# Kernel optimization log

Measured on AMD Instinct MI355X. Metric: run time of the kernel, lower is better.

Reference implementation:

```python
import jax, jax.numpy as jnp
import numpy as np
import math

N, L, C, H, K = 4, 16384, 256, 8, 4
D = C // H


def setup_inputs():
    rng = jax.random.key(0)
    ks = jax.random.split(rng, 16)
    def w(k, shape, scale):
        return jax.random.normal(k, shape, jnp.float32) * scale
    s = 1.0 / math.sqrt(C)
    return {
        "query": jax.random.normal(ks[0], (N, L, C), jnp.float32),
        "key": jax.random.normal(ks[1], (N, L, C), jnp.float32),
        "value": jax.random.normal(ks[2], (N, L, C), jnp.float32),
        "reference_points": jax.random.uniform(ks[3], (N, L, 2), jnp.float32),
        "pos_embed": jax.random.normal(ks[4], (N, L, C), jnp.float32),
        "Wq": w(ks[5], (C, C), s), "bq": jnp.zeros((C,), jnp.float32),
        "Wk": w(ks[6], (C, C), s), "bk": jnp.zeros((C,), jnp.float32),
        "Wv": w(ks[7], (C, C), s), "bv": jnp.zeros((C,), jnp.float32),
        "Wo1": w(ks[8], (C, 2 * C), s), "bo1": jnp.zeros((2 * C,), jnp.float32),
        "Wo2": w(ks[9], (2 * C, H * K * 2), 0.02), "bo2": w(ks[10], (H * K * 2,), 0.02),
        "Wpos": w(ks[11], (C, C), s), "bpos": jnp.zeros((C,), jnp.float32),
        "Wout": w(ks[12], (C, C), s), "bout": jnp.zeros((C,), jnp.float32),
    }


def _sample_weight(points):
    # F.grid_sample on a 1x1 feature map (bilinear, zeros padding, align_corners=False)
    # degenerates to a scalar weight: grid g = 2p-1, unnormalized c = g/2 = p - 0.5,
    # pixel-0 bilinear weight per axis = max(0, 1 - |c|).
    c = points - 0.5
    return jax.nn.relu(1.0 - jnp.abs(c[..., 0])) * jax.nn.relu(1.0 - jnp.abs(c[..., 1]))


def reference(query, key, value, reference_points, pos_embed,
              Wq, bq, Wk, bk, Wv, bv, Wo1, bo1, Wo2, bo2, Wpos, bpos, Wout, bout):
    Nb, Ln, Cd = query.shape
    q = (query @ Wq + bq).reshape(Nb, Ln, H, D)
    k = (key @ Wk + bk).reshape(Nb, Ln, H, D)
    v = (value @ Wv + bv).reshape(Nb, Ln, H, D)
    pos = (pos_embed @ Wpos + bpos).reshape(Nb, Ln, H, D)
    q = q + pos
    k = k + pos
    # offset MLP: Linear(C,2C) -> ReLU -> Linear(2C, H*K*2)
    offsets = (jax.nn.relu(query @ Wo1 + bo1) @ Wo2 + bo2).reshape(Nb, Ln, H, K, 2)
    sp = reference_points[:, :, None, None, :] + offsets  # [N,L,H,K,2]
    w = _sample_weight(sp)                                # [N,L,H,K]
    # sampled_k[n,l,h,k,:] = k[n,l,h,:] * w[n,l,h,k]  (1x1 grid_sample closed form)
    qk = jnp.einsum('nlhd,nlhd->nlh', q, k)               # [N,L,H]
    attn = jax.nn.softmax(qk[..., None] * w / math.sqrt(D), axis=-1)  # [N,L,H,K]
    # output = sum_k attn_k * (v * w_k) = v * sum_k(attn_k * w_k)
    wv = jnp.sum(attn * w, axis=-1)                       # [N,L,H]
    out = (v * wv[..., None]).reshape(Nb, Ln, Cd)
    return out @ Wout + bout
```

## Files before the change

kernel.cpp:

```cpp
#include <hip/hip_runtime.h>
#include <hip/hip_bf16.h>

typedef __bf16 bf16x8 __attribute__((ext_vector_type(8)));
typedef float f32x4 __attribute__((ext_vector_type(4)));
typedef float f32x2 __attribute__((ext_vector_type(2)));

#define MT 64
#define CC 256

__device__ __forceinline__ void barrier_lds() {
    __builtin_amdgcn_sched_barrier(0);
    asm volatile("s_waitcnt lgkmcnt(0)" ::: "memory");
    __builtin_amdgcn_s_barrier();
    __builtin_amdgcn_sched_barrier(0);
}

__device__ __forceinline__ int swz(int r, int c) {
    return r * 512 + ((c * 2) ^ ((r & 7) << 4));
}

__device__ __forceinline__ bf16x8 ldB(const __bf16* __restrict__ WT, int nc, int KC, int kc,
                                      int laneoff) {
    return *(const bf16x8*)(WT + ((size_t)nc * KC + kc) * 512 + laneoff);
}

__device__ __forceinline__ void stream_tile(const float* __restrict__ src, int row0, int tid,
                                            __bf16* dst) {
#pragma unroll
    for (int i = 0; i < 8; ++i) {
        int f = i * 512 + tid;
        int r = f >> 6;
        int c = (f & 63) * 4;
        f32x4 v = __builtin_nontemporal_load((const f32x4*)(src + (size_t)(row0 + r) * CC + c));
        union { __bf16 h[4]; unsigned long long u; } uu;
        uu.h[0] = (__bf16)v[0]; uu.h[1] = (__bf16)v[1];
        uu.h[2] = (__bf16)v[2]; uu.h[3] = (__bf16)v[3];
        *(unsigned long long*)((char*)dst + swz(r, c)) = uu.u;
    }
}

__global__ void prep_all(const float* __restrict__ Wq, const float* __restrict__ Wk,
                         const float* __restrict__ Wpos, const float* __restrict__ Wo1,
                         const float* __restrict__ Wo2, const float* __restrict__ Wv,
                         const float* __restrict__ Wout, __bf16* __restrict__ ws)
{
    int i = blockIdx.x * 256 + threadIdx.x;
    if (i >= 557056) return;
    int j, K, N;
    const float* S0 = nullptr; const float* S1 = nullptr;
    if (i < 131072)      { j = i;          K = 512; N = 256; S0 = Wq;  S1 = Wpos; }
    else if (i < 262144) { j = i - 131072; K = 512; N = 256; S0 = Wk;  S1 = Wpos; }
    else if (i < 393216) { j = i - 262144; K = 256; N = 512; S0 = Wo1; }
    else if (i < 425984) { j = i - 393216; K = 512; N = 64;  S0 = Wo2; }
    else if (i < 491520) { j = i - 425984; K = 256; N = 256; S0 = Wv; }
    else                 { j = i - 491520; K = 256; N = 256; S0 = Wout; }
    int tile = j >> 9, r = j & 511;
    int lane = r >> 3, e = r & 7;
    int q4 = lane >> 4, r16 = lane & 15;
    int KC = K >> 5;
    int nc = tile / KC, kc = tile - nc * KC;
    int k = kc * 32 + q4 * 8 + e;
    int n = nc * 16 + r16;
    float v;
    if (S1 && k >= 256) v = S1[(size_t)(k - 256) * N + n];
    else                v = S0[(size_t)k * N + n];
    ws[i] = (__bf16)v;
}

extern "C" __global__ void __launch_bounds__(512, 2)
fused_ext_attn(const float* __restrict__ query, const float* __restrict__ key,
               const float* __restrict__ value, const float* __restrict__ refp,
               const float* __restrict__ pose,
               const __bf16* __restrict__ ws,
               const float* __restrict__ bq, const float* __restrict__ bk,
               const float* __restrict__ bv, const float* __restrict__ bpos,
               const float* __restrict__ bo1, const float* __restrict__ bo2,
               const float* __restrict__ bout,
               float* __restrict__ out)
{
    const __bf16* WTqp  = ws;
    const __bf16* WTkp  = ws + 131072;
    const __bf16* WTo1  = ws + 262144;
    const __bf16* WTo2  = ws + 393216;
    const __bf16* WTv   = ws + 425984;
    const __bf16* WTout = ws + 491520;

    __shared__ __attribute__((aligned(16))) __bf16 SA[MT * CC];
    __shared__ __attribute__((aligned(16))) __bf16 SX[MT * CC];
    __shared__ __attribute__((aligned(16))) char   SY[12288];

    __bf16* off_b = (__bf16*)SY;
    float*  qk_s  = (float*)(SY + 8192);
    float*  wv_s  = (float*)(SY + 10240);

    const int tid = threadIdx.x;
    const int lane = tid & 63;
    const int wid = tid >> 6;
    const int r16 = lane & 15;
    const int q4 = lane >> 4;
    const int laneoff = lane * 8;
    const int row0 = blockIdx.x * MT;

    stream_tile(query, row0, tid, SA);
    barrier_lds();

    f32x4 accO[4];
#pragma unroll
    for (int i = 0; i < 4; ++i) accO[i] = (f32x4){0.f, 0.f, 0.f, 0.f};
    for (int p = 0; p < 2; ++p) {
        f32x4 acc[4][2];
#pragma unroll
        for (int i = 0; i < 4; ++i)
#pragma unroll
            for (int j = 0; j < 2; ++j) acc[i][j] = (f32x4){0.f, 0.f, 0.f, 0.f};
#pragma unroll
        for (int ks = 0; ks < 8; ++ks) {
            int ak = ks * 32 + q4 * 8;
            bf16x8 a[4], b[2];
#pragma unroll
            for (int mf = 0; mf < 4; ++mf)
                a[mf] = *(const bf16x8*)((const char*)SA + swz(mf * 16 + r16, ak));
#pragma unroll
            for (int nf = 0; nf < 2; ++nf)
                b[nf] = ldB(WTo1, p * 16 + wid * 2 + nf, 8, ks, laneoff);
#pragma unroll
            for (int mf = 0; mf < 4; ++mf)
#pragma unroll
                for (int nf = 0; nf < 2; ++nf)
                    acc[mf][nf] = __builtin_amdgcn_mfma_f32_16x16x32_bf16(a[mf], b[nf], acc[mf][nf], 0, 0, 0);
        }
#pragma unroll
        for (int mf = 0; mf < 4; ++mf)
#pragma unroll
            for (int nf = 0; nf < 2; ++nf) {
                int col = wid * 32 + nf * 16 + r16;
                float bias = bo1[p * 256 + col];
#pragma unroll
                for (int r = 0; r < 4; ++r)
                    *(__bf16*)((char*)SX + swz(mf * 16 + q4 * 4 + r, col)) =
                        (__bf16)fmaxf(acc[mf][nf][r] + bias, 0.f);
            }
        barrier_lds();
        if (wid < 4) {
#pragma unroll
            for (int ks = 0; ks < 8; ++ks) {
                int ak = ks * 32 + q4 * 8;
                bf16x8 b = ldB(WTo2, wid, 16, p * 8 + ks, laneoff);
#pragma unroll
                for (int mf = 0; mf < 4; ++mf) {
                    bf16x8 a = *(const bf16x8*)((const char*)SX + swz(mf * 16 + r16, ak));
                    accO[mf] = __builtin_amdgcn_mfma_f32_16x16x32_bf16(a, b, accO[mf], 0, 0, 0);
                }
            }
            if (p == 1) {
                int col = wid * 16 + r16;
                float b2 = bo2[col];
#pragma unroll
                for (int mf = 0; mf < 4; ++mf)
#pragma unroll
                    for (int r = 0; r < 4; ++r)
                        off_b[(mf * 16 + q4 * 4 + r) * 64 + col] = (__bf16)(accO[mf][r] + b2);
            }
        }
        barrier_lds();
    }

    f32x4 qa[4][2];
#pragma unroll
    for (int i = 0; i < 4; ++i)
#pragma unroll
        for (int j = 0; j < 2; ++j) qa[i][j] = (f32x4){0.f, 0.f, 0.f, 0.f};
    stream_tile(pose, row0, tid, SX);
#pragma unroll
    for (int ks = 0; ks < 8; ++ks) {
        int ak = ks * 32 + q4 * 8;
        bf16x8 a[4], b[2];
#pragma unroll
        for (int mf = 0; mf < 4; ++mf)
            a[mf] = *(const bf16x8*)((const char*)SA + swz(mf * 16 + r16, ak));
#pragma unroll
        for (int nf = 0; nf < 2; ++nf)
            b[nf] = ldB(WTqp, wid * 2 + nf, 16, ks, laneoff);
#pragma unroll
        for (int mf = 0; mf < 4; ++mf)
#pragma unroll
            for (int nf = 0; nf < 2; ++nf)
                qa[mf][nf] = __builtin_amdgcn_mfma_f32_16x16x32_bf16(a[mf], b[nf], qa[mf][nf], 0, 0, 0);
    }
    barrier_lds();

    stream_tile(key, row0, tid, SA);
#pragma unroll
    for (int ks = 8; ks < 16; ++ks) {
        int ak = (ks - 8) * 32 + q4 * 8;
        bf16x8 a[4], b[2];
#pragma unroll
        for (int mf = 0; mf < 4; ++mf)
            a[mf] = *(const bf16x8*)((const char*)SX + swz(mf * 16 + r16, ak));
#pragma unroll
        for (int nf = 0; nf < 2; ++nf)
            b[nf] = ldB(WTqp, wid * 2 + nf, 16, ks, laneoff);
#pragma unroll
        for (int mf = 0; mf < 4; ++mf)
#pragma unroll
            for (int nf = 0; nf < 2; ++nf)
                qa[mf][nf] = __builtin_amdgcn_mfma_f32_16x16x32_bf16(a[mf], b[nf], qa[mf][nf], 0, 0, 0);
    }
    barrier_lds();

    {
        f32x4 ka[4][2];
#pragma unroll
        for (int i = 0; i < 4; ++i)
#pragma unroll
            for (int j = 0; j < 2; ++j) ka[i][j] = (f32x4){0.f, 0.f, 0.f, 0.f};
#pragma unroll
        for (int ks = 0; ks < 16; ++ks) {
            int ak = (ks & 7) * 32 + q4 * 8;
            const char* Abase = (ks < 8) ? (const char*)SA : (const char*)SX;
            bf16x8 a[4], b[2];
#pragma unroll
            for (int mf = 0; mf < 4; ++mf)
                a[mf] = *(const bf16x8*)(Abase + swz(mf * 16 + r16, ak));
#pragma unroll
            for (int nf = 0; nf < 2; ++nf)
                b[nf] = ldB(WTkp, wid * 2 + nf, 16, ks, laneoff);
#pragma unroll
            for (int mf = 0; mf < 4; ++mf)
#pragma unroll
                for (int nf = 0; nf < 2; ++nf)
                    ka[mf][nf] = __builtin_amdgcn_mfma_f32_16x16x32_bf16(a[mf], b[nf], ka[mf][nf], 0, 0, 0);
        }
        float Bq[2], Bk[2];
#pragma unroll
        for (int nf = 0; nf < 2; ++nf) {
            int col = wid * 32 + nf * 16 + r16;
            Bq[nf] = bq[col] + bpos[col];
            Bk[nf] = bk[col] + bpos[col];
        }
#pragma unroll
        for (int mf = 0; mf < 4; ++mf)
#pragma unroll
            for (int r = 0; r < 4; ++r) {
                float p0 = (qa[mf][0][r] + Bq[0]) * (ka[mf][0][r] + Bk[0])
                         + (qa[mf][1][r] + Bq[1]) * (ka[mf][1][r] + Bk[1]);
#pragma unroll
                for (int m = 1; m < 16; m <<= 1)
                    p0 += __shfl_xor(p0, m);
                if (r16 == 0)
                    qk_s[(mf * 16 + q4 * 4 + r) * 8 + wid] = p0;
            }
    }
    barrier_lds();

    stream_tile(value, row0, tid, SA);
    {
        int t = tid >> 3, h = tid & 7;
        float qk = qk_s[t * 8 + h];
        f32x2 rp = __builtin_nontemporal_load((const f32x2*)(refp + (size_t)(row0 + t) * 2));
        float wgt[4], lg[4];
        float m = -1e30f;
#pragma unroll
        for (int kk = 0; kk < 4; ++kk) {
            float ox = (float)off_b[t * 64 + (h * 4 + kk) * 2];
            float oy = (float)off_b[t * 64 + (h * 4 + kk) * 2 + 1];
            float cx = rp[0] + ox - 0.5f, cy = rp[1] + oy - 0.5f;
            float wx = fmaxf(0.f, 1.f - fabsf(cx));
            float wy = fmaxf(0.f, 1.f - fabsf(cy));
            wgt[kk] = wx * wy;
            lg[kk] = qk * wgt[kk] * 0.17677669529663687f;
            m = fmaxf(m, lg[kk]);
        }
        float s = 0.f, sw = 0.f;
#pragma unroll
        for (int kk = 0; kk < 4; ++kk) {
            float e = __expf(lg[kk] - m);
            s += e;
            sw += e * wgt[kk];
        }
        wv_s[t * 8 + h] = sw / s;
    }
    barrier_lds();

    {
        f32x4 acc[4][2];
#pragma unroll
        for (int i = 0; i < 4; ++i)
#pragma unroll
            for (int j = 0; j < 2; ++j) acc[i][j] = (f32x4){0.f, 0.f, 0.f, 0.f};
#pragma unroll
        for (int ks = 0; ks < 8; ++ks) {
            int ak = ks * 32 + q4 * 8;
            bf16x8 a[4], b[2];
#pragma unroll
            for (int mf = 0; mf < 4; ++mf)
                a[mf] = *(const bf16x8*)((const char*)SA + swz(mf * 16 + r16, ak));
#pragma unroll
            for (int nf = 0; nf < 2; ++nf)
                b[nf] = ldB(WTv, wid * 2 + nf, 8, ks, laneoff);
#pragma unroll
            for (int mf = 0; mf < 4; ++mf)
#pragma unroll
                for (int nf = 0; nf < 2; ++nf)
                    acc[mf][nf] = __builtin_amdgcn_mfma_f32_16x16x32_bf16(a[mf], b[nf], acc[mf][nf], 0, 0, 0);
        }
#pragma unroll
        for (int mf = 0; mf < 4; ++mf)
#pragma unroll
            for (int nf = 0; nf < 2; ++nf) {
                int col = wid * 32 + nf * 16 + r16;
                float bias = bv[col];
#pragma unroll
                for (int r = 0; r < 4; ++r) {
                    int row = mf * 16 + q4 * 4 + r;
                    float wvv = wv_s[row * 8 + wid];
                    *(__bf16*)((char*)SX + swz(row, col)) = (__bf16)((acc[mf][nf][r] + bias) * wvv);
                }
            }
    }
    barrier_lds();

    {
        f32x4 acc[4][2];
#pragma unroll
        for (int i = 0; i < 4; ++i)
#pragma unroll
            for (int j = 0; j < 2; ++j) acc[i][j] = (f32x4){0.f, 0.f, 0.f, 0.f};
#pragma unroll
        for (int ks = 0; ks < 8; ++ks) {
            int ak = ks * 32 + q4 * 8;
            bf16x8 a[4], b[2];
#pragma unroll
            for (int mf = 0; mf < 4; ++mf)
                a[mf] = *(const bf16x8*)((const char*)SX + swz(mf * 16 + r16, ak));
#pragma unroll
            for (int nf = 0; nf < 2; ++nf)
                b[nf] = ldB(WTout, wid * 2 + nf, 8, ks, laneoff);
#pragma unroll
            for (int mf = 0; mf < 4; ++mf)
#pragma unroll
                for (int nf = 0; nf < 2; ++nf)
                    acc[mf][nf] = __builtin_amdgcn_mfma_f32_16x16x32_bf16(a[mf], b[nf], acc[mf][nf], 0, 0, 0);
        }
#pragma unroll
        for (int mf = 0; mf < 4; ++mf)
#pragma unroll
            for (int nf = 0; nf < 2; ++nf) {
                int col = wid * 32 + nf * 16 + r16;
                float bias = bout[col];
#pragma unroll
                for (int r = 0; r < 4; ++r) {
                    int row = mf * 16 + q4 * 4 + r;
                    __builtin_nontemporal_store(acc[mf][nf][r] + bias,
                                                out + (size_t)(row0 + row) * CC + col);
                }
            }
    }
}

extern "C" void kernel_launch(void* const* d_in, const int* in_sizes, int n_in,
                              void* d_out, int out_size, void* d_ws, size_t ws_size,
                              hipStream_t stream)
{
    const float* query = (const float*)d_in[0];
    const float* key   = (const float*)d_in[1];
    const float* value = (const float*)d_in[2];
    const float* refp  = (const float*)d_in[3];
    const float* pose  = (const float*)d_in[4];
    const float* Wq  = (const float*)d_in[5];  const float* bq   = (const float*)d_in[6];
    const float* Wk  = (const float*)d_in[7];  const float* bk   = (const float*)d_in[8];
    const float* Wv  = (const float*)d_in[9];  const float* bv   = (const float*)d_in[10];
    const float* Wo1 = (const float*)d_in[11]; const float* bo1  = (const float*)d_in[12];
    const float* Wo2 = (const float*)d_in[13]; const float* bo2  = (const float*)d_in[14];
    const float* Wpos= (const float*)d_in[15]; const float* bpos = (const float*)d_in[16];
    const float* Wout= (const float*)d_in[17]; const float* bout = (const float*)d_in[18];

    __bf16* ws = (__bf16*)d_ws;

    prep_all<<<2176, 256, 0, stream>>>(Wq, Wk, Wpos, Wo1, Wo2, Wv, Wout, ws);

    fused_ext_attn<<<65536 / MT, 512, 0, stream>>>(
        query, key, value, refp, pose, ws,
        bq, bk, bv, bpos, bo1, bo2, bout, (float*)d_out);
}
```

Before: 140.4 us.

## Prefetch next GEMM weight fragments into registers ahead of each stage

Each stage's weight B-fragments (a full 8x2 set of bf16x8 per wave) are now loaded into registers before the preceding barrier or right after the previous GEMM, so global weight loads overlap with LDS stores, barriers and the tile streaming. The offset-MLP loop is unrolled into explicit stages, with the second-layer weights preloaded. To hold the larger register footprint, launch bounds drop from 2 to 1 block per CU, which cuts occupancy and may expose latency elsewhere.

```diff
diff --git a/kernel.cpp b/kernel.cpp
--- a/kernel.cpp
+++ b/kernel.cpp
@@ -22,6 +22,38 @@
 __device__ __forceinline__ bf16x8 ldB(const __bf16* __restrict__ WT, int nc, int KC, int kc,
                                       int laneoff) {
     return *(const bf16x8*)(WT + ((size_t)nc * KC + kc) * 512 + laneoff);
+}
+
+__device__ __forceinline__ void pre16(bf16x8 (&d)[8][2], const __bf16* __restrict__ WT,
+                                      int nc0, int KC, int kc0, int laneoff) {
+#pragma unroll
+    for (int ks = 0; ks < 8; ++ks)
+#pragma unroll
+        for (int nf = 0; nf < 2; ++nf)
+            d[ks][nf] = ldB(WT, nc0 + nf, KC, kc0 + ks, laneoff);
+}
+__device__ __forceinline__ void pre8(bf16x8 (&d)[8], const __bf16* __restrict__ WT,
+                                     int nc, int KC, int kc0, int laneoff) {
+#pragma unroll
+    for (int ks = 0; ks < 8; ++ks)
+        d[ks] = ldB(WT, nc, KC, kc0 + ks, laneoff);
+}
+
+__device__ __forceinline__ void gemm16(const char* A, const bf16x8 (&b)[8][2],
+                                       f32x4 (&acc)[4][2], int r16, int q4) {
+#pragma unroll
+    for (int ks = 0; ks < 8; ++ks) {
+        int ak = ks * 32 + q4 * 8;
+        bf16x8 a[4];
+#pragma unroll
+        for (int mf = 0; mf < 4; ++mf)
+            a[mf] = *(const bf16x8*)(A + swz(mf * 16 + r16, ak));
+#pragma unroll
+        for (int mf = 0; mf < 4; ++mf)
+#pragma unroll
+            for (int nf = 0; nf < 2; ++nf)
+                acc[mf][nf] = __builtin_amdgcn_mfma_f32_16x16x32_bf16(a[mf], b[ks][nf], acc[mf][nf], 0, 0, 0);
+    }
 }
 
 __device__ __forceinline__ void stream_tile(const float* __restrict__ src, int row0, int tid,
@@ -67,7 +99,7 @@
     ws[i] = (__bf16)v;
 }
 
-extern "C" __global__ void __launch_bounds__(512, 2)
+extern "C" __global__ void __launch_bounds__(512, 1)
 fused_ext_attn(const float* __restrict__ query, const float* __restrict__ key,
                const float* __restrict__ value, const float* __restrict__ refp,
                const float* __restrict__ pose,
@@ -101,69 +133,94 @@
     const int laneoff = lane * 8;
     const int row0 = blockIdx.x * MT;
 
+    bf16x8 bh[8][2];
     stream_tile(query, row0, tid, SA);
+    pre16(bh, WTo1, wid * 2, 8, 0, laneoff);
     barrier_lds();
 
     f32x4 accO[4];
 #pragma unroll
     for (int i = 0; i < 4; ++i) accO[i] = (f32x4){0.f, 0.f, 0.f, 0.f};
-    for (int p = 0; p < 2; ++p) {
+    bf16x8 bo[8];
+    {
         f32x4 acc[4][2];
 #pragma unroll
         for (int i = 0; i < 4; ++i)
 #pragma unroll
             for (int j = 0; j < 2; ++j) acc[i][j] = (f32x4){0.f, 0.f, 0.f, 0.f};
-#pragma unroll
-        for (int ks = 0; ks < 8; ++ks) {
-            int ak = ks * 32 + q4 * 8;
-            bf16x8 a[4], b[2];
-#pragma unroll
-            for (int mf = 0; mf < 4; ++mf)
-                a[mf] = *(const bf16x8*)((const char*)SA + swz(mf * 16 + r16, ak));
-#pragma unroll
-            for (int nf = 0; nf < 2; ++nf)
-                b[nf] = ldB(WTo1, p * 16 + wid * 2 + nf, 8, ks, laneoff);
-#pragma unroll
-            for (int mf = 0; mf < 4; ++mf)
-#pragma unroll
-                for (int nf = 0; nf < 2; ++nf)
-                    acc[mf][nf] = __builtin_amdgcn_mfma_f32_16x16x32_bf16(a[mf], b[nf], acc[mf][nf], 0, 0, 0);
-        }
+        gemm16((const char*)SA, bh, acc, r16, q4);
+        pre8(bo, WTo2, wid & 3, 16, 0, laneoff);
 #pragma unroll
         for (int mf = 0; mf < 4; ++mf)
 #pragma unroll
             for (int nf = 0; nf < 2; ++nf) {
                 int col = wid * 32 + nf * 16 + r16;
-                float bias = bo1[p * 256 + col];
+                float bias = bo1[col];
 #pragma unroll
                 for (int r = 0; r < 4; ++r)
                     *(__bf16*)((char*)SX + swz(mf * 16 + q4 * 4 + r, col)) =
                         (__bf16)fmaxf(acc[mf][nf][r] + bias, 0.f);
             }
-        barrier_lds();
-        if (wid < 4) {
-#pragma unroll
-            for (int ks = 0; ks < 8; ++ks) {
-                int ak = ks * 32 + q4 * 8;
-                bf16x8 b = ldB(WTo2, wid, 16, p * 8 + ks, laneoff);
-#pragma unroll
-                for (int mf = 0; mf < 4; ++mf) {
-                    bf16x8 a = *(const bf16x8*)((const char*)SX + swz(mf * 16 + r16, ak));
-                    accO[mf] = __builtin_amdgcn_mfma_f32_16x16x32_bf16(a, b, accO[mf], 0, 0, 0);
-                }
-            }
-            if (p == 1) {
-                int col = wid * 16 + r16;
-                float b2 = bo2[col];
-#pragma unroll
-                for (int mf = 0; mf < 4; ++mf)
-#pragma unroll
-                    for (int r = 0; r < 4; ++r)
-                        off_b[(mf * 16 + q4 * 4 + r) * 64 + col] = (__bf16)(accO[mf][r] + b2);
-            }
-        }
-        barrier_lds();
-    }
+    }
+    barrier_lds();
+
+    if (wid < 4) {
+#pragma unroll
+        for (int ks = 0; ks < 8; ++ks) {
+            int ak = ks * 32 + q4 * 8;
+#pragma unroll
+            for (int mf = 0; mf < 4; ++mf) {
+                bf16x8 a = *(const bf16x8*)((const char*)SX + swz(mf * 16 + r16, ak));
+                accO[mf] = __builtin_amdgcn_mfma_f32_16x16x32_bf16(a, bo[ks], accO[mf], 0, 0, 0);
+            }
+        }
+    }
+    pre16(bh, WTo1, 16 + wid * 2, 8, 0, laneoff);
+    barrier_lds();
+
+    {
+        f32x4 acc[4][2];
+#pragma unroll
+        for (int i = 0; i < 4; ++i)
+#pragma unroll
+            for (int j = 0; j < 2; ++j) acc[i][j] = (f32x4){0.f, 0.f, 0.f, 0.f};
+        gemm16((const char*)SA, bh, acc, r16, q4);
+        pre8(bo, WTo2, wid & 3, 16, 8, laneoff);
+#pragma unroll
+        for (int mf = 0; mf < 4; ++mf)
+#pragma unroll
+            for (int nf = 0; nf < 2; ++nf) {
+                int col = wid * 32 + nf * 16 + r16;
+                float bias = bo1[256 + col];
+#pragma unroll
+                for (int r = 0; r < 4; ++r)
+                    *(__bf16*)((char*)SX + swz(mf * 16 + q4 * 4 + r, col)) =
+                        (__bf16)fmaxf(acc[mf][nf][r] + bias, 0.f);
+            }
+    }
+    barrier_lds();
+
+    bf16x8 bg[8][2];
+    if (wid < 4) {
+#pragma unroll
+        for (int ks = 0; ks < 8; ++ks) {
+            int ak = ks * 32 + q4 * 8;
+#pragma unroll
+            for (int mf = 0; mf < 4; ++mf) {
+                bf16x8 a = *(const bf16x8*)((const char*)SX + swz(mf * 16 + r16, ak));
+                accO[mf] = __builtin_amdgcn_mfma_f32_16x16x32_bf16(a, bo[ks], accO[mf], 0, 0, 0);
+            }
+        }
+        int col = (wid & 3) * 16 + r16;
+        float b2 = bo2[col];
+#pragma unroll
+        for (int mf = 0; mf < 4; ++mf)
+#pragma unroll
+            for (int r = 0; r < 4; ++r)
+                off_b[(mf * 16 + q4 * 4 + r) * 64 + col] = (__bf16)(accO[mf][r] + b2);
+    }
+    pre16(bg, WTqp, wid * 2, 16, 0, laneoff);
+    barrier_lds();
 
     f32x4 qa[4][2];
 #pragma unroll
@@ -171,41 +228,14 @@
 #pragma unroll
         for (int j = 0; j < 2; ++j) qa[i][j] = (f32x4){0.f, 0.f, 0.f, 0.f};
     stream_tile(pose, row0, tid, SX);
-#pragma unroll
-    for (int ks = 0; ks < 8; ++ks) {
-        int ak = ks * 32 + q4 * 8;
-        bf16x8 a[4], b[2];
-#pragma unroll
-        for (int mf = 0; mf < 4; ++mf)
-            a[mf] = *(const bf16x8*)((const char*)SA + swz(mf * 16 + r16, ak));
-#pragma unroll
-        for (int nf = 0; nf < 2; ++nf)
-            b[nf] = ldB(WTqp, wid * 2 + nf, 16, ks, laneoff);
-#pragma unroll
-        for (int mf = 0; mf < 4; ++mf)
-#pragma unroll
-            for (int nf = 0; nf < 2; ++nf)
-                qa[mf][nf] = __builtin_amdgcn_mfma_f32_16x16x32_bf16(a[mf], b[nf], qa[mf][nf], 0, 0, 0);
-    }
-    barrier_lds();
-
+    gemm16((const char*)SA, bg, qa, r16, q4);
+    pre16(bg, WTqp, wid * 2, 16, 8, laneoff);
+    barrier_lds();
+
+    bf16x8 bk1[8][2];
     stream_tile(key, row0, tid, SA);
-#pragma unroll
-    for (int ks = 8; ks < 16; ++ks) {
-        int ak = (ks - 8) * 32 + q4 * 8;
-        bf16x8 a[4], b[2];
-#pragma unroll
-        for (int mf = 0; mf < 4; ++mf)
-            a[mf] = *(const bf16x8*)((const char*)SX + swz(mf * 16 + r16, ak));
-#pragma unroll
-        for (int nf = 0; nf < 2; ++nf)
-            b[nf] = ldB(WTqp, wid * 2 + nf, 16, ks, laneoff);
-#pragma unroll
-        for (int mf = 0; mf < 4; ++mf)
-#pragma unroll
-            for (int nf = 0; nf < 2; ++nf)
-                qa[mf][nf] = __builtin_amdgcn_mfma_f32_16x16x32_bf16(a[mf], b[nf], qa[mf][nf], 0, 0, 0);
-    }
+    gemm16((const char*)SX, bg, qa, r16, q4);
+    pre16(bk1, WTkp, wid * 2, 16, 0, laneoff);
     barrier_lds();
 
     {
@@ -214,14 +244,14 @@
         for (int i = 0; i < 4; ++i)
 #pragma unroll
             for (int j = 0; j < 2; ++j) ka[i][j] = (f32x4){0.f, 0.f, 0.f, 0.f};
-#pragma unroll
-        for (int ks = 0; ks < 16; ++ks) {
-            int ak = (ks & 7) * 32 + q4 * 8;
-            const char* Abase = (ks < 8) ? (const char*)SA : (const char*)SX;
+        gemm16((const char*)SA, bk1, ka, r16, q4);
+#pragma unroll
+        for (int ks = 8; ks < 16; ++ks) {
+            int ak = (ks - 8) * 32 + q4 * 8;
             bf16x8 a[4], b[2];
 #pragma unroll
             for (int mf = 0; mf < 4; ++mf)
-                a[mf] = *(const bf16x8*)(Abase + swz(mf * 16 + r16, ak));
+                a[mf] = *(const bf16x8*)((const char*)SX + swz(mf * 16 + r16, ak));
 #pragma unroll
             for (int nf = 0; nf < 2; ++nf)
                 b[nf] = ldB(WTkp, wid * 2 + nf, 16, ks, laneoff);
@@ -231,6 +261,7 @@
                 for (int nf = 0; nf < 2; ++nf)
                     ka[mf][nf] = __builtin_amdgcn_mfma_f32_16x16x32_bf16(a[mf], b[nf], ka[mf][nf], 0, 0, 0);
         }
+        pre16(bg, WTv, wid * 2, 8, 0, laneoff);
         float Bq[2], Bk[2];
 #pragma unroll
         for (int nf = 0; nf < 2; ++nf) {
@@ -288,22 +319,8 @@
         for (int i = 0; i < 4; ++i)
 #pragma unroll
             for (int j = 0; j < 2; ++j) acc[i][j] = (f32x4){0.f, 0.f, 0.f, 0.f};
-#pragma unroll
-        for (int ks = 0; ks < 8; ++ks) {
-            int ak = ks * 32 + q4 * 8;
-            bf16x8 a[4], b[2];
-#pragma unroll
-            for (int mf = 0; mf < 4; ++mf)
-                a[mf] = *(const bf16x8*)((const char*)SA + swz(mf * 16 + r16, ak));
-#pragma unroll
-            for (int nf = 0; nf < 2; ++nf)
-                b[nf] = ldB(WTv, wid * 2 + nf, 8, ks, laneoff);
-#pragma unroll
-            for (int mf = 0; mf < 4; ++mf)
-#pragma unroll
-                for (int nf = 0; nf < 2; ++nf)
-                    acc[mf][nf] = __builtin_amdgcn_mfma_f32_16x16x32_bf16(a[mf], b[nf], acc[mf][nf], 0, 0, 0);
-        }
+        gemm16((const char*)SA, bg, acc, r16, q4);
+        pre16(bh, WTout, wid * 2, 8, 0, laneoff);
 #pragma unroll
         for (int mf = 0; mf < 4; ++mf)
 #pragma unroll
@@ -326,22 +343,7 @@
         for (int i = 0; i < 4; ++i)
 #pragma unroll
             for (int j = 0; j < 2; ++j) acc[i][j] = (f32x4){0.f, 0.f, 0.f, 0.f};
-#pragma unroll
-        for (int ks = 0; ks < 8; ++ks) {
-            int ak = ks * 32 + q4 * 8;
-            bf16x8 a[4], b[2];
-#pragma unroll
-            for (int mf = 0; mf < 4; ++mf)
-                a[mf] = *(const bf16x8*)((const char*)SX + swz(mf * 16 + r16, ak));
-#pragma unroll
-            for (int nf = 0; nf < 2; ++nf)
-                b[nf] = ldB(WTout, wid * 2 + nf, 8, ks, laneoff);
-#pragma unroll
-            for (int mf = 0; mf < 4; ++mf)
-#pragma unroll
-                for (int nf = 0; nf < 2; ++nf)
-                    acc[mf][nf] = __builtin_amdgcn_mfma_f32_16x16x32_bf16(a[mf], b[nf], acc[mf][nf], 0, 0, 0);
-        }
+        gemm16((const char*)SX, bh, acc, r16, q4);
 #pragma unroll
         for (int mf = 0; mf < 4; ++mf)
 #pragma unroll
```

Result: slower. 152.3 us (+8.4%).
